# Kernel optimization log

Measured on AMD Instinct MI355X. Metric: run time of the kernel, lower is better.

Reference implementation:

```python
import jax, jax.numpy as jnp
import numpy as np

D_MODEL = 1024
NHEAD = 16
HEAD_DIM = D_MODEL // NHEAD


def setup_inputs() -> dict:
    key = jax.random.key(0)
    ks = jax.random.split(key, 9)
    B, T = 2, 2048
    s = 1.0 / np.sqrt(D_MODEL)
    return {
        "sequence": jax.random.normal(ks[0], (B, T, D_MODEL), dtype=jnp.float32),
        "wq": jax.random.normal(ks[1], (D_MODEL, D_MODEL), dtype=jnp.float32) * s,
        "bq": jax.random.normal(ks[2], (D_MODEL,), dtype=jnp.float32) * 0.01,
        "wk": jax.random.normal(ks[3], (D_MODEL, D_MODEL), dtype=jnp.float32) * s,
        "bk": jax.random.normal(ks[4], (D_MODEL,), dtype=jnp.float32) * 0.01,
        "wv": jax.random.normal(ks[5], (D_MODEL, D_MODEL), dtype=jnp.float32) * s,
        "bv": jax.random.normal(ks[6], (D_MODEL,), dtype=jnp.float32) * 0.01,
        "wo": jax.random.normal(ks[7], (D_MODEL, D_MODEL), dtype=jnp.float32) * s,
        "bo": jax.random.normal(ks[8], (D_MODEL,), dtype=jnp.float32) * 0.01,
    }


def reference(sequence, wq, bq, wk, bk, wv, bv, wo, bo):
    B, T, C = sequence.shape
    scale = jnp.asarray(HEAD_DIM ** 0.5, sequence.dtype)
    # projections (nn.Linear: x @ W.T + b)
    def proj(x, w, b):
        y = x @ w.T + b
        return y.reshape(B, T, NHEAD, HEAD_DIM).transpose(0, 2, 1, 3)  # [B,H,T,Dh]
    q = proj(sequence, wq, bq)
    k = proj(sequence, wk, bk)
    v = proj(sequence, wv, bv)
    scores = jnp.einsum("bhqd,bhkd->bhqk", q, k) / scale
    causal = jnp.tril(jnp.ones((T, T), dtype=bool))
    scores = jnp.where(causal, scores, jnp.asarray(-jnp.inf, scores.dtype))
    attn = jax.nn.softmax(scores, axis=-1)
    out = jnp.einsum("bhqk,bhkd->bhqd", attn, v)
    out = out.transpose(0, 2, 1, 3).reshape(B, T, C)
    return out @ wo.T + bo
```

## Files before the change

kernel.cpp:

```cpp
#include <hip/hip_runtime.h>
#include <hip/hip_bf16.h>
#include <hip/hip_fp16.h>
#include <type_traits>

#define DM 1024
#define NH 16
#define HD 64
#define BATCH 2
#define SEQ 2048
#define MROWS (BATCH*SEQ)

typedef __hip_bfloat16 bf16;
typedef __attribute__((ext_vector_type(8))) short    bf16x8;
typedef __attribute__((ext_vector_type(8))) short    s16x8;
typedef __attribute__((ext_vector_type(8))) _Float16 f16x8;
typedef __attribute__((ext_vector_type(4))) _Float16 f16x4;
typedef __attribute__((ext_vector_type(4))) short    s16x4;
typedef __attribute__((ext_vector_type(4))) float    f32x4;

#define LOG2E 1.44269504f
#define M_FIX 4.0f

__device__ __forceinline__ short f2bf(float x) {
    union { float f; unsigned u; } v; v.f = x;
    unsigned r = v.u + 0x7FFF + ((v.u >> 16) & 1);
    return (short)(r >> 16);
}

__device__ __forceinline__ bf16x8 ld8f(const float* p) {
    const float4 a = *(const float4*)p;
    const float4 b = *(const float4*)(p + 4);
    bf16x8 r;
    r[0]=f2bf(a.x); r[1]=f2bf(a.y); r[2]=f2bf(a.z); r[3]=f2bf(a.w);
    r[4]=f2bf(b.x); r[5]=f2bf(b.y); r[6]=f2bf(b.z); r[7]=f2bf(b.w);
    return r;
}

__device__ __forceinline__ void gload_lds16(const void* g, void* l) {
    __builtin_amdgcn_global_load_lds(
        (const __attribute__((address_space(1))) void*)g,
        (__attribute__((address_space(3))) void*)l, 16, 0, 0);
}

__global__ __launch_bounds__(256)
void cvt_bf16(const float* __restrict__ s0, const float* __restrict__ s1,
              const float* __restrict__ s2, const float* __restrict__ s3,
              const float* __restrict__ s4,
              short* d0, short* d1, short* d2, short* d3, short* d4)
{
    const int y = blockIdx.y;
    const float* src = (y==0? s0 : y==1? s1 : y==2? s2 : y==3? s3 : s4);
    short*       dst = (y==0? d0 : y==1? d1 : y==2? d2 : y==3? d3 : d4);
    const int n = (y == 0) ? MROWS*DM : DM*DM;
    const int i = (blockIdx.x * 256 + threadIdx.x) * 8;
    if (i < n) *(bf16x8*)(dst + i) = ld8f(src + i);
}

template<int MODE>
__device__ __forceinline__
void gemm_epilogue(f32x4 (&acc)[4][4], const float* bi, void* out, int z,
                   int tile_m, int tile_n, int wm, int wn,
                   int fr, int quad, int lane, short* lA)
{
    if (MODE == 1 && z == 2) {
        __syncthreads();
        short* sc = lA + (int)(threadIdx.x >> 6) * 256;
        const int rd = lane >> 2, tc = lane & 3;
        #pragma unroll
        for (int mi = 0; mi < 4; ++mi) {
            #pragma unroll
            for (int ni = 0; ni < 4; ++ni) {
                const int colg = tile_n + wn + ni*16 + fr;
                const float bia = bi[colg];
                f16x4 w;
                #pragma unroll
                for (int r = 0; r < 4; ++r) w[r] = (_Float16)(acc[mi][ni][r] + bia);
                *(f16x4*)(sc + fr*16 + quad*4) = w;
                const f16x4 vv = *(const f16x4*)(sc + rd*16 + tc*4);
                const int dg = tile_n + wn + ni*16 + rd;
                const int tg = tile_m + wm + mi*16 + tc*4;
                const int hh = dg >> 6, dd = dg & (HD-1);
                const int bb = tg >> 11, tt = tg & (SEQ-1);
                const int kt = tt >> 5, tko = tt & 31;
                *(f16x4*)((_Float16*)out +
                    ((((size_t)(bb*NH + hh))*(SEQ/32) + kt)*HD + dd)*32 + tko) = vv;
            }
        }
    } else {
        #pragma unroll
        for (int mi = 0; mi < 4; ++mi) {
            #pragma unroll
            for (int ni = 0; ni < 4; ++ni) {
                const int colg = tile_n + wn + ni*16 + fr;
                const float bia = bi[colg];
                #pragma unroll
                for (int r = 0; r < 4; ++r) {
                    const int rowg = tile_m + wm + mi*16 + quad*4 + r;
                    const float v = acc[mi][ni][r] + bia;
                    if (MODE == 0) {
                        ((float*)out)[(size_t)rowg*DM + colg] = v;
                    } else {
                        const int bb = rowg >> 11, t = rowg & (SEQ-1);
                        const int h  = colg >> 6,  d = colg & (HD-1);
                        ((_Float16*)out)[(((size_t)(bb*NH + h))*SEQ + t)*HD + d] = (_Float16)v;
                    }
                }
            }
        }
    }
}

template<int MODE>
__global__ __launch_bounds__(256)
void gemm_a(const short* __restrict__ A,
            const short* __restrict__ W0, const short* __restrict__ W1, const short* __restrict__ W2,
            const float* __restrict__ b0, const float* __restrict__ b1, const float* __restrict__ b2,
            void* o0, void* o1, void* o2)
{
    __shared__ __align__(16) short lA[128*32];
    __shared__ __align__(16) short lB[128*32];

    const int tid  = threadIdx.x;
    const int wid  = tid >> 6;
    const int lane = tid & 63;
    const int tile_n = blockIdx.x * 128;
    const int tile_m = blockIdx.y * 128;
    const int z = blockIdx.z;

    const short* Wg = (z == 0 ? W0 : (z == 1 ? W1 : W2));
    const float* bi = (z == 0 ? b0 : (z == 1 ? b1 : b2));
    void*        out = (z == 0 ? o0 : (z == 1 ? o1 : o2));

    const int sa_row = tile_m + wid*32 + (lane >> 2);
    const int sb_row = tile_n + wid*32 + (lane >> 2);
    const int scol   = (lane & 3) * 8;
    short* lA0 = lA + wid*1024 + lane*8;
    short* lA1 = lA0 + 512;
    short* lB0 = lB + wid*1024 + lane*8;
    short* lB1 = lB0 + 512;

    const int wm = (wid >> 1) * 64;
    const int wn = (wid & 1) * 64;
    const int fr = lane & 15;
    const int quad = lane >> 4;
    const int fq = quad * 8;

    f32x4 acc[4][4] = {};

    for (int k0 = 0; k0 < DM; k0 += 32) {
        __syncthreads();
        gload_lds16(A  + (size_t)sa_row*DM      + k0 + scol, lA0);
        gload_lds16(A  + (size_t)(sa_row+16)*DM + k0 + scol, lA1);
        gload_lds16(Wg + (size_t)sb_row*DM      + k0 + scol, lB0);
        gload_lds16(Wg + (size_t)(sb_row+16)*DM + k0 + scol, lB1);
        __syncthreads();

        bf16x8 af[4], bfv[4];
        #pragma unroll
        for (int i = 0; i < 4; ++i) af[i]  = *(const bf16x8*)(lA + (wm + i*16 + fr)*32 + fq);
        #pragma unroll
        for (int i = 0; i < 4; ++i) bfv[i] = *(const bf16x8*)(lB + (wn + i*16 + fr)*32 + fq);

        #pragma unroll
        for (int mi = 0; mi < 4; ++mi)
            #pragma unroll
            for (int ni = 0; ni < 4; ++ni)
                acc[mi][ni] = __builtin_amdgcn_mfma_f32_16x16x32_bf16(
                    af[mi], bfv[ni], acc[mi][ni], 0, 0, 0);
    }
    gemm_epilogue<MODE>(acc, bi, out, z, tile_m, tile_n, wm, wn, fr, quad, lane, lA);
}

template<typename TA, int MODE>
__global__ __launch_bounds__(256)
void gemm_f(const TA* __restrict__ A,
            const float* __restrict__ W0, const float* __restrict__ W1, const float* __restrict__ W2,
            const float* __restrict__ b0, const float* __restrict__ b1, const float* __restrict__ b2,
            void* o0, void* o1, void* o2)
{
    __shared__ __align__(16) short lA[128*32];
    __shared__ __align__(16) short lB[128*32];

    const int tid  = threadIdx.x;
    const int wid  = tid >> 6;
    const int lane = tid & 63;
    const int tile_n = blockIdx.x * 128;
    const int tile_m = blockIdx.y * 128;
    const int z = blockIdx.z;

    const float* Wg = (z == 0 ? W0 : (z == 1 ? W1 : W2));
    const float* bi = (z == 0 ? b0 : (z == 1 ? b1 : b2));
    void*        out = (z == 0 ? o0 : (z == 1 ? o1 : o2));

    const int sa_row = tile_m + wid*32 + (lane >> 2);
    const int sb_row = tile_n + wid*32 + (lane >> 2);
    const int scol   = (lane & 3) * 8;
    short* lA0 = lA + wid*1024 + lane*8;
    short* lA1 = lA0 + 512;
    short* lB0 = lB + wid*1024 + lane*8;
    short* lB1 = lB0 + 512;

    const int wm = (wid >> 1) * 64;
    const int wn = (wid & 1) * 64;
    const int fr = lane & 15;
    const int quad = lane >> 4;
    const int fq = quad * 8;

    f32x4 acc[4][4] = {};

    for (int k0 = 0; k0 < DM; k0 += 32) {
        bf16x8 ra0, ra1;
        if constexpr (std::is_same<TA, float>::value) {
            ra0 = ld8f((const float*)A + (size_t)sa_row*DM      + k0 + scol);
            ra1 = ld8f((const float*)A + (size_t)(sa_row+16)*DM + k0 + scol);
        } else {
            ra0 = *(const bf16x8*)((const short*)A + (size_t)sa_row*DM      + k0 + scol);
            ra1 = *(const bf16x8*)((const short*)A + (size_t)(sa_row+16)*DM + k0 + scol);
        }
        const bf16x8 rb0 = ld8f(Wg + (size_t)sb_row*DM      + k0 + scol);
        const bf16x8 rb1 = ld8f(Wg + (size_t)(sb_row+16)*DM + k0 + scol);

        __syncthreads();
        *(bf16x8*)lA0 = ra0;
        *(bf16x8*)lA1 = ra1;
        *(bf16x8*)lB0 = rb0;
        *(bf16x8*)lB1 = rb1;
        __syncthreads();

        bf16x8 af[4], bfv[4];
        #pragma unroll
        for (int i = 0; i < 4; ++i) af[i]  = *(const bf16x8*)(lA + (wm + i*16 + fr)*32 + fq);
        #pragma unroll
        for (int i = 0; i < 4; ++i) bfv[i] = *(const bf16x8*)(lB + (wn + i*16 + fr)*32 + fq);

        #pragma unroll
        for (int mi = 0; mi < 4; ++mi)
            #pragma unroll
            for (int ni = 0; ni < 4; ++ni)
                acc[mi][ni] = __builtin_amdgcn_mfma_f32_16x16x32_bf16(
                    af[mi], bfv[ni], acc[mi][ni], 0, 0, 0);
    }
    gemm_epilogue<MODE>(acc, bi, out, z, tile_m, tile_n, wm, wn, fr, quad, lane, lA);
}

__global__ __launch_bounds__(256)
void attn(const _Float16* __restrict__ Q, const _Float16* __restrict__ K,
          const _Float16* __restrict__ Vt, short* __restrict__ O)
{
    __shared__ __align__(16) _Float16 lsK[2][2048];
    __shared__ __align__(16) _Float16 lsV[2][2048];

    const int t    = threadIdx.x;
    const int lane = t & 63;
    const int wid  = t >> 6;
    const int id   = blockIdx.x;
    const int bh   = id & 31;
    const int s    = id >> 5;
    const int sq_  = s >> 3, sr_ = s & 7;
    const int band = (sq_ == 0) ? sr_ : (sq_ == 1) ? 15 - sr_
                   : (sq_ == 2) ? 16 + sr_ : 31 - sr_;

    const size_t base = (size_t)bh * SEQ * HD;
    const int qr = lane & 15;
    const int quad = lane >> 4;
    const int bb = bh >> 4, h = bh & (NH-1);

    const int k_goff = ((t>>2)&31)*64 + (t>>7)*32 + (t&3)*8;
    const int v_goff = (t&63)*32 + (t>>6)*8;

    const float SC1 = 0.125f * LOG2E;
    const float SC2 = -M_FIX * LOG2E;
    const int vboff = (quad>>1)*512 + (quad&1)*4 + qr*8;

    const int q_tile = band*64 + wid*16;
    const int q_idx  = q_tile + qr;
    const int ntiles = 2*band + 2;
    const int ktm    = 2*band + (wid >> 1);

    const f16x8* Qv = (const f16x8*)(Q + base + (size_t)(q_tile + qr)*HD);
    const f16x8 qf0 = Qv[quad];
    const f16x8 qf1 = Qv[quad + 4];

    float l_cur = 0.f;
    f32x4 o[4] = {};

    gload_lds16(K  + base + k_goff, &lsK[0][0] + t*8);
    gload_lds16(Vt + base + v_goff, &lsV[0][0] + t*8);

    int cur = 0;
    #pragma unroll 1
    for (int kt = 0; kt < ntiles; ++kt) {
        if (kt + 1 < ntiles) {
            gload_lds16(K  + base + (size_t)(kt+1)*2048 + k_goff, &lsK[cur^1][0] + t*8);
            gload_lds16(Vt + base + (size_t)(kt+1)*2048 + v_goff, &lsV[cur^1][0] + t*8);
            asm volatile("s_waitcnt vmcnt(2)" ::: "memory");
        } else {
            asm volatile("s_waitcnt vmcnt(0)" ::: "memory");
        }
        __builtin_amdgcn_s_barrier();
        __builtin_amdgcn_sched_barrier(0);

        if (kt <= ktm) {
            const _Float16* sK = &lsK[cur][0];
            const _Float16* sV = &lsV[cur][0];

            const f16x8 ka0 = *(const f16x8*)(sK + qr*32 + quad*8);
            const f16x8 ka1 = *(const f16x8*)(sK + 1024 + qr*32 + quad*8);
            const f16x8 kb0 = *(const f16x8*)(sK + (16+qr)*32 + quad*8);
            const f16x8 kb1 = *(const f16x8*)(sK + 1024 + (16+qr)*32 + quad*8);

            __builtin_amdgcn_s_setprio(1);
            f32x4 s0 = {}, s1 = {};
            s0 = __builtin_amdgcn_mfma_f32_16x16x32_f16(ka0, qf0, s0, 0, 0, 0);
            s0 = __builtin_amdgcn_mfma_f32_16x16x32_f16(ka1, qf1, s0, 0, 0, 0);
            s1 = __builtin_amdgcn_mfma_f32_16x16x32_f16(kb0, qf0, s1, 0, 0, 0);
            s1 = __builtin_amdgcn_mfma_f32_16x16x32_f16(kb1, qf1, s1, 0, 0, 0);

            f16x4 p0, p1;
            const int k_base = kt*32;
            if (kt == ktm) {
                #pragma unroll
                for (int r = 0; r < 4; ++r) {
                    const int key = k_base + quad*4 + r;
                    float e0 = exp2f(s0[r] * SC1 + SC2);
                    float e1 = exp2f(s1[r] * SC1 + SC2);
                    e0 = (key      <= q_idx) ? e0 : 0.f;
                    e1 = (key + 16 <= q_idx) ? e1 : 0.f;
                    l_cur += e0 + e1;
                    p0[r] = (_Float16)e0;
                    p1[r] = (_Float16)e1;
                }
            } else {
                #pragma unroll
                for (int r = 0; r < 4; ++r) {
                    const float e0 = exp2f(s0[r] * SC1 + SC2);
                    const float e1 = exp2f(s1[r] * SC1 + SC2);
                    l_cur += e0 + e1;
                    p0[r] = (_Float16)e0;
                    p1[r] = (_Float16)e1;
                }
            }

            #pragma unroll
            for (int dt = 0; dt < 4; ++dt) {
                const f16x4 av0 = *(const f16x4*)(sV + vboff + dt*128);
                const f16x4 av1 = *(const f16x4*)(sV + 1024 + vboff + dt*128);
                o[dt] = __builtin_amdgcn_mfma_f32_16x16x16f16(av0, p0, o[dt], 0, 0, 0);
                o[dt] = __builtin_amdgcn_mfma_f32_16x16x16f16(av1, p1, o[dt], 0, 0, 0);
            }
            __builtin_amdgcn_s_setprio(0);
        }
        __builtin_amdgcn_sched_barrier(0);
        __builtin_amdgcn_s_barrier();
        cur ^= 1;
    }

    l_cur += __shfl_xor(l_cur, 16, 64);
    l_cur += __shfl_xor(l_cur, 32, 64);
    const float linv = 1.0f / fmaxf(l_cur, 1e-30f);

    const int tq = q_tile + qr;
    #pragma unroll
    for (int dt = 0; dt < 4; ++dt) {
        s16x4 pk;
        #pragma unroll
        for (int r = 0; r < 4; ++r) pk[r] = f2bf(o[dt][r] * linv);
        *(s16x4*)(O + ((size_t)(bb*SEQ + tq))*DM + h*HD + dt*16 + quad*4) = pk;
    }
}

extern "C" void kernel_launch(void* const* d_in, const int* in_sizes, int n_in,
                              void* d_out, int out_size, void* d_ws, size_t ws_size,
                              hipStream_t stream)
{
    const float* seq = (const float*)d_in[0];
    const float* wq  = (const float*)d_in[1];
    const float* bq  = (const float*)d_in[2];
    const float* wk  = (const float*)d_in[3];
    const float* bk  = (const float*)d_in[4];
    const float* wv  = (const float*)d_in[5];
    const float* bv  = (const float*)d_in[6];
    const float* wo  = (const float*)d_in[7];
    const float* bo  = (const float*)d_in[8];

    _Float16* Qb = (_Float16*)d_ws;
    _Float16* Kb = Qb + (size_t)MROWS*DM;
    _Float16* Vt = Kb + (size_t)MROWS*DM;
    short*    Ob = (short*)(Vt + (size_t)MROWS*DM);
    short*    sq16 = Ob + (size_t)MROWS*DM;
    short*    wq16 = sq16 + (size_t)MROWS*DM;
    short*    wk16 = wq16 + (size_t)DM*DM;
    short*    wv16 = wk16 + (size_t)DM*DM;
    short*    wo16 = wv16 + (size_t)DM*DM;

    const size_t need = ((size_t)MROWS*DM*2)*5 + ((size_t)DM*DM*2)*4;
    const bool fast = ws_size >= need;

    if (fast) {
        dim3 gc(MROWS*DM/(256*8), 5, 1);
        cvt_bf16<<<gc, 256, 0, stream>>>(seq, wq, wk, wv, wo,
                                         sq16, wq16, wk16, wv16, wo16);

        dim3 g1(DM/128, MROWS/128, 3);
        gemm_a<1><<<g1, 256, 0, stream>>>(sq16, wq16, wk16, wv16, bq, bk, bv,
                                          (void*)Qb, (void*)Kb, (void*)Vt);

        attn<<<dim3(1024), 256, 0, stream>>>(Qb, Kb, Vt, Ob);

        dim3 g3(DM/128, MROWS/128, 1);
        gemm_a<0><<<g3, 256, 0, stream>>>(Ob, wo16, wo16, wo16, bo, bo, bo,
                                          d_out, d_out, d_out);
    } else {
        dim3 g1(DM/128, MROWS/128, 3);
        gemm_f<float, 1><<<g1, 256, 0, stream>>>(seq, wq, wk, wv, bq, bk, bv,
                                                 (void*)Qb, (void*)Kb, (void*)Vt);

        attn<<<dim3(1024), 256, 0, stream>>>(Qb, Kb, Vt, Ob);

        dim3 g3(DM/128, MROWS/128, 1);
        gemm_f<short, 0><<<g3, 256, 0, stream>>>(Ob, wo, wo, wo, bo, bo, bo,
                                                 d_out, d_out, d_out);
    }
}
```

Before: 206.7 us.

## Pair complementary causal bands per block and double K/V tile size

Each attention block now processes two query bands, xb and 31-xb, one after the other, so every block does a balanced amount of causal work. The grid is halved to 512 blocks. Each pipeline stage also loads a 64-key K/V tile instead of 32, halving the number of barrier and wait rounds. The cost is less parallelism (512 blocks on a large GPU), double the LDS per block which may reduce occupancy, and a K/V pipeline refill at the start of the second band.

```diff
diff --git a/kernel.cpp b/kernel.cpp
--- a/kernel.cpp
+++ b/kernel.cpp
@@ -247,19 +247,15 @@
 void attn(const _Float16* __restrict__ Q, const _Float16* __restrict__ K,
           const _Float16* __restrict__ Vt, short* __restrict__ O)
 {
-    __shared__ __align__(16) _Float16 lsK[2][2048];
-    __shared__ __align__(16) _Float16 lsV[2][2048];
+    __shared__ __align__(16) _Float16 lsK[2][4096];
+    __shared__ __align__(16) _Float16 lsV[2][4096];
 
     const int t    = threadIdx.x;
     const int lane = t & 63;
     const int wid  = t >> 6;
     const int id   = blockIdx.x;
     const int bh   = id & 31;
-    const int s    = id >> 5;
-    const int sq_  = s >> 3, sr_ = s & 7;
-    const int band = (sq_ == 0) ? sr_ : (sq_ == 1) ? 15 - sr_
-                   : (sq_ == 2) ? 16 + sr_ : 31 - sr_;
-
+    const int xb   = id >> 5;
     const size_t base = (size_t)bh * SEQ * HD;
     const int qr = lane & 15;
     const int quad = lane >> 4;
@@ -272,100 +268,119 @@
     const float SC2 = -M_FIX * LOG2E;
     const int vboff = (quad>>1)*512 + (quad&1)*4 + qr*8;
 
-    const int q_tile = band*64 + wid*16;
-    const int q_idx  = q_tile + qr;
-    const int ntiles = 2*band + 2;
-    const int ktm    = 2*band + (wid >> 1);
-
-    const f16x8* Qv = (const f16x8*)(Q + base + (size_t)(q_tile + qr)*HD);
-    const f16x8 qf0 = Qv[quad];
-    const f16x8 qf1 = Qv[quad + 4];
-
-    float l_cur = 0.f;
-    f32x4 o[4] = {};
-
-    gload_lds16(K  + base + k_goff, &lsK[0][0] + t*8);
-    gload_lds16(Vt + base + v_goff, &lsV[0][0] + t*8);
-
-    int cur = 0;
     #pragma unroll 1
-    for (int kt = 0; kt < ntiles; ++kt) {
-        if (kt + 1 < ntiles) {
-            gload_lds16(K  + base + (size_t)(kt+1)*2048 + k_goff, &lsK[cur^1][0] + t*8);
-            gload_lds16(Vt + base + (size_t)(kt+1)*2048 + v_goff, &lsV[cur^1][0] + t*8);
-            asm volatile("s_waitcnt vmcnt(2)" ::: "memory");
-        } else {
-            asm volatile("s_waitcnt vmcnt(0)" ::: "memory");
-        }
-        __builtin_amdgcn_s_barrier();
-        __builtin_amdgcn_sched_barrier(0);
-
-        if (kt <= ktm) {
-            const _Float16* sK = &lsK[cur][0];
-            const _Float16* sV = &lsV[cur][0];
-
-            const f16x8 ka0 = *(const f16x8*)(sK + qr*32 + quad*8);
-            const f16x8 ka1 = *(const f16x8*)(sK + 1024 + qr*32 + quad*8);
-            const f16x8 kb0 = *(const f16x8*)(sK + (16+qr)*32 + quad*8);
-            const f16x8 kb1 = *(const f16x8*)(sK + 1024 + (16+qr)*32 + quad*8);
-
-            __builtin_amdgcn_s_setprio(1);
-            f32x4 s0 = {}, s1 = {};
-            s0 = __builtin_amdgcn_mfma_f32_16x16x32_f16(ka0, qf0, s0, 0, 0, 0);
-            s0 = __builtin_amdgcn_mfma_f32_16x16x32_f16(ka1, qf1, s0, 0, 0, 0);
-            s1 = __builtin_amdgcn_mfma_f32_16x16x32_f16(kb0, qf0, s1, 0, 0, 0);
-            s1 = __builtin_amdgcn_mfma_f32_16x16x32_f16(kb1, qf1, s1, 0, 0, 0);
-
-            f16x4 p0, p1;
-            const int k_base = kt*32;
-            if (kt == ktm) {
-                #pragma unroll
-                for (int r = 0; r < 4; ++r) {
-                    const int key = k_base + quad*4 + r;
-                    float e0 = exp2f(s0[r] * SC1 + SC2);
-                    float e1 = exp2f(s1[r] * SC1 + SC2);
-                    e0 = (key      <= q_idx) ? e0 : 0.f;
-                    e1 = (key + 16 <= q_idx) ? e1 : 0.f;
-                    l_cur += e0 + e1;
-                    p0[r] = (_Float16)e0;
-                    p1[r] = (_Float16)e1;
-                }
+    for (int half = 0; half < 2; ++half) {
+        const int band = half ? (31 - xb) : xb;
+        const int q_tile = band*64 + wid*16;
+        const int q_idx  = q_tile + qr;
+        const int NT     = band + 1;
+        const int ktm    = 2*band + (wid >> 1);
+
+        const f16x8* Qv = (const f16x8*)(Q + base + (size_t)q_idx*HD);
+        const f16x8 qf0 = Qv[quad];
+        const f16x8 qf1 = Qv[quad + 4];
+
+        float l_cur = 0.f;
+        f32x4 o[4] = {};
+
+        gload_lds16(K  + base + k_goff,        &lsK[0][0]    + t*8);
+        gload_lds16(K  + base + 2048 + k_goff, &lsK[0][2048] + t*8);
+        gload_lds16(Vt + base + v_goff,        &lsV[0][0]    + t*8);
+        gload_lds16(Vt + base + 2048 + v_goff, &lsV[0][2048] + t*8);
+
+        int cur = 0;
+        #pragma unroll 1
+        for (int u = 0; u < NT; ++u) {
+            if (u + 1 < NT) {
+                const size_t g = base + (size_t)(u+1)*4096;
+                _Float16* dK = &lsK[cur^1][0] + t*8;
+                _Float16* dV = &lsV[cur^1][0] + t*8;
+                gload_lds16(K  + g + k_goff,        dK);
+                gload_lds16(K  + g + 2048 + k_goff, dK + 2048);
+                gload_lds16(Vt + g + v_goff,        dV);
+                gload_lds16(Vt + g + 2048 + v_goff, dV + 2048);
+                asm volatile("s_waitcnt vmcnt(4)" ::: "memory");
             } else {
-                #pragma unroll
-                for (int r = 0; r < 4; ++r) {
-                    const float e0 = exp2f(s0[r] * SC1 + SC2);
-                    const float e1 = exp2f(s1[r] * SC1 + SC2);
-                    l_cur += e0 + e1;
-                    p0[r] = (_Float16)e0;
-                    p1[r] = (_Float16)e1;
+                asm volatile("s_waitcnt vmcnt(0)" ::: "memory");
+            }
+            __builtin_amdgcn_s_barrier();
+            __builtin_amdgcn_sched_barrier(0);
+
+            #pragma unroll
+            for (int s2 = 0; s2 < 2; ++s2) {
+                const int kt32 = 2*u + s2;
+                if (kt32 <= ktm) {
+                    const _Float16* sK = &lsK[cur][s2*2048];
+                    const _Float16* sV = &lsV[cur][s2*2048];
+
+                    const f16x8 ka0 = *(const f16x8*)(sK + qr*32 + quad*8);
+                    const f16x8 ka1 = *(const f16x8*)(sK + 1024 + qr*32 + quad*8);
+                    const f16x8 kb0 = *(const f16x8*)(sK + (16+qr)*32 + quad*8);
+                    const f16x8 kb1 = *(const f16x8*)(sK + 1024 + (16+qr)*32 + quad*8);
+
+                    __builtin_amdgcn_s_setprio(1);
+                    f32x4 s0 = {}, s1 = {};
+                    s0 = __builtin_amdgcn_mfma_f32_16x16x32_f16(ka0, qf0, s0, 0, 0, 0);
+                    s0 = __builtin_amdgcn_mfma_f32_16x16x32_f16(ka1, qf1, s0, 0, 0, 0);
+                    s1 = __builtin_amdgcn_mfma_f32_16x16x32_f16(kb0, qf0, s1, 0, 0, 0);
+                    s1 = __builtin_amdgcn_mfma_f32_16x16x32_f16(kb1, qf1, s1, 0, 0, 0);
+
+                    f16x4 p0, p1;
+                    const int k_base = kt32*32;
+                    if (kt32 == ktm) {
+                        float ls = 0.f;
+                        #pragma unroll
+                        for (int r = 0; r < 4; ++r) {
+                            const int key = k_base + quad*4 + r;
+                            float e0 = exp2f(s0[r] * SC1 + SC2);
+                            float e1 = exp2f(s1[r] * SC1 + SC2);
+                            e0 = (key      <= q_idx) ? e0 : 0.f;
+                            e1 = (key + 16 <= q_idx) ? e1 : 0.f;
+                            ls += e0 + e1;
+                            p0[r] = (_Float16)e0;
+                            p1[r] = (_Float16)e1;
+                        }
+                        l_cur += ls;
+                    } else {
+                        float ls = 0.f;
+                        #pragma unroll
+                        for (int r = 0; r < 4; ++r) {
+                            const float e0 = exp2f(s0[r] * SC1 + SC2);
+                            const float e1 = exp2f(s1[r] * SC1 + SC2);
+                            ls += e0 + e1;
+                            p0[r] = (_Float16)e0;
+                            p1[r] = (_Float16)e1;
+                        }
+                        l_cur += ls;
+                    }
+
+                    #pragma unroll
+                    for (int dt = 0; dt < 4; ++dt) {
+                        const f16x4 av0 = *(const f16x4*)(sV + vboff + dt*128);
+                        const f16x4 av1 = *(const f16x4*)(sV + 1024 + vboff + dt*128);
+                        o[dt] = __builtin_amdgcn_mfma_f32_16x16x16f16(av0, p0, o[dt], 0, 0, 0);
+                        o[dt] = __builtin_amdgcn_mfma_f32_16x16x16f16(av1, p1, o[dt], 0, 0, 0);
+                    }
+                    __builtin_amdgcn_s_setprio(0);
                 }
             }
-
-            #pragma unroll
-            for (int dt = 0; dt < 4; ++dt) {
-                const f16x4 av0 = *(const f16x4*)(sV + vboff + dt*128);
-                const f16x4 av1 = *(const f16x4*)(sV + 1024 + vboff + dt*128);
-                o[dt] = __builtin_amdgcn_mfma_f32_16x16x16f16(av0, p0, o[dt], 0, 0, 0);
-                o[dt] = __builtin_amdgcn_mfma_f32_16x16x16f16(av1, p1, o[dt], 0, 0, 0);
-            }
-            __builtin_amdgcn_s_setprio(0);
+            __builtin_amdgcn_sched_barrier(0);
+            __builtin_amdgcn_s_barrier();
+            cur ^= 1;
         }
-        __builtin_amdgcn_sched_barrier(0);
-        __builtin_amdgcn_s_barrier();
-        cur ^= 1;
-    }
-
-    l_cur += __shfl_xor(l_cur, 16, 64);
-    l_cur += __shfl_xor(l_cur, 32, 64);
-    const float linv = 1.0f / fmaxf(l_cur, 1e-30f);
-
-    const int tq = q_tile + qr;
-    #pragma unroll
-    for (int dt = 0; dt < 4; ++dt) {
-        s16x4 pk;
-        #pragma unroll
-        for (int r = 0; r < 4; ++r) pk[r] = f2bf(o[dt][r] * linv);
-        *(s16x4*)(O + ((size_t)(bb*SEQ + tq))*DM + h*HD + dt*16 + quad*4) = pk;
+
+        l_cur += __shfl_xor(l_cur, 16, 64);
+        l_cur += __shfl_xor(l_cur, 32, 64);
+        const float linv = 1.0f / fmaxf(l_cur, 1e-30f);
+
+        const int tq = q_tile + qr;
+        #pragma unroll
+        for (int dt = 0; dt < 4; ++dt) {
+            s16x4 pk;
+            #pragma unroll
+            for (int r = 0; r < 4; ++r) pk[r] = f2bf(o[dt][r] * linv);
+            *(s16x4*)(O + ((size_t)(bb*SEQ + tq))*DM + h*HD + dt*16 + quad*4) = pk;
+        }
     }
 }
 
@@ -405,7 +420,7 @@
         gemm_a<1><<<g1, 256, 0, stream>>>(sq16, wq16, wk16, wv16, bq, bk, bv,
                                           (void*)Qb, (void*)Kb, (void*)Vt);
 
-        attn<<<dim3(1024), 256, 0, stream>>>(Qb, Kb, Vt, Ob);
+        attn<<<dim3(512), 256, 0, stream>>>(Qb, Kb, Vt, Ob);
 
         dim3 g3(DM/128, MROWS/128, 1);
         gemm_a<0><<<g3, 256, 0, stream>>>(Ob, wo16, wo16, wo16, bo, bo, bo,
@@ -415,7 +430,7 @@
         gemm_f<float, 1><<<g1, 256, 0, stream>>>(seq, wq, wk, wv, bq, bk, bv,
                                                  (void*)Qb, (void*)Kb, (void*)Vt);
 
-        attn<<<dim3(1024), 256, 0, stream>>>(Qb, Kb, Vt, Ob);
+        attn<<<dim3(512), 256, 0, stream>>>(Qb, Kb, Vt, Ob);
 
         dim3 g3(DM/128, MROWS/128, 1);
         gemm_f<short, 0><<<g3, 256, 0, stream>>>(Ob, wo, wo, wo, bo, bo, bo,
```

Result: faster. 198.4 us (-4.0%).
